# Kernel tuning notes

Measured on AMD Instinct MI355X. Metric: run time of the kernel, lower is better.

## Reference

```python
import math
import jax, jax.numpy as jnp
import numpy as np

N_HEADS = 16
D_EMBED = 1024
D_HEAD = D_EMBED // N_HEADS


def setup_inputs() -> dict:
    key = jax.random.key(0)
    k1, k2, k3, k4, k5 = jax.random.split(key, 5)
    B, S, D = 4, 2048, D_EMBED
    scale = 1.0 / math.sqrt(D)
    return {
        "x": jax.random.normal(k1, (B, S, D), dtype=jnp.float32),
        "in_proj_w": jax.random.normal(k2, (3 * D, D), dtype=jnp.float32) * scale,
        "in_proj_b": jax.random.normal(k3, (3 * D,), dtype=jnp.float32) * 0.02,
        "out_proj_w": jax.random.normal(k4, (D, D), dtype=jnp.float32) * scale,
        "out_proj_b": jax.random.normal(k5, (D,), dtype=jnp.float32) * 0.02,
        "causal_mask": 0,
    }


def reference(x, in_proj_w, in_proj_b, out_proj_w, out_proj_b, causal_mask):
    B, S, D = x.shape
    # in_proj: torch Linear -> x @ W^T + b, then chunk into q,k,v
    qkv = x @ in_proj_w.T + in_proj_b              # [B,S,3D]
    q, k, v = jnp.split(qkv, 3, axis=-1)
    # [B,S,D] -> [B,H,S,d]
    def heads(t):
        return t.reshape(B, S, N_HEADS, D_HEAD).transpose(0, 2, 1, 3)
    q, k, v = heads(q), heads(k), heads(v)
    weight = jnp.einsum("bhsd,bhtd->bhst", q, k)   # [B,H,S,S] materialized scores
    if causal_mask:
        mask = jnp.triu(jnp.ones((S, S), dtype=bool), k=1)
        weight = jnp.where(mask, -jnp.inf, weight)
    weight = jax.nn.softmax(weight / math.sqrt(D_HEAD), axis=-1)
    out = jnp.einsum("bhst,bhtd->bhsd", weight, v)  # [B,H,S,d]
    out = out.transpose(0, 2, 1, 3).reshape(B, S, D)
    return out @ out_proj_w.T + out_proj_b
```

## Files before the change

kernel.cpp:

```cpp
#include <hip/hip_runtime.h>

typedef unsigned short u16;
typedef _Float16 h8 __attribute__((ext_vector_type(8)));
typedef __fp16 fp16x2 __attribute__((ext_vector_type(2)));
typedef float f32x4 __attribute__((ext_vector_type(4)));

constexpr int B_ = 4, S_ = 2048, D_ = 1024, H_ = 16;

__device__ __forceinline__ void async16(const void* g, void* l) {
  __builtin_amdgcn_global_load_lds(
      (const __attribute__((address_space(1))) void*)g,
      (__attribute__((address_space(3))) void*)l, 16, 0, 0);
}

__device__ __forceinline__ unsigned pk2(float a, float b) {
  union { fp16x2 h; unsigned u; } c;
  c.h = __builtin_amdgcn_cvt_pkrtz(a, b);
  return c.u;
}

__global__ __launch_bounds__(256) void cvt3_kernel(
    const float* __restrict__ x, const float* __restrict__ wi,
    const float* __restrict__ wo, _Float16* __restrict__ xh,
    _Float16* __restrict__ wih, _Float16* __restrict__ woh)
{
  const int bid = blockIdx.x;
  const float* src;
  _Float16* dst;
  int base;
  if (bid < 8192)       { src = x;  dst = xh;  base = bid; }
  else if (bid < 11264) { src = wi; dst = wih; base = bid - 8192; }
  else                  { src = wo; dst = woh; base = bid - 11264; }
  const int i = (base * 256 + threadIdx.x) * 4;
  const float4 v = *(const float4*)(src + i);
  uint2 o;
  o.x = pk2(v.x, v.y);
  o.y = pk2(v.z, v.w);
  *(uint2*)(dst + i) = o;
}

template<bool OUT_HALF, int BPW>
__global__ __launch_bounds__(512, 2) void gemm256d_f16(
    const _Float16* __restrict__ A, const _Float16* __restrict__ Bw,
    const float* __restrict__ bias, void* __restrict__ Cout,
    int M, int N, int K)
{
  constexpr int BN = BPW * 64;
  constexpr int NBB = BN / 8;
  __shared__ __align__(16) _Float16 sA[2][16384];
  __shared__ __align__(16) _Float16 sB[2][NBB * 512];

  const int tid = threadIdx.x;
  const int lane = tid & 63, w = tid >> 6;
  const int wm = w >> 2, wn = w & 3;

  const int id = blockIdx.x;
  const int cpx = gridDim.x >> 3;
  const int swz = (id & 7) * cpx + (id >> 3);
  const int nbx = N / BN;
  const int bx = swz % nbx, by = swz / nbx;
  const int m0 = by * 256, n0 = bx * BN;

  const int r15 = lane & 15, s4 = lane >> 4;
  const _Float16* gA[4];
  int loA[4];
#pragma unroll
  for (int j = 0; j < 4; ++j) {
    const int t = 2 * w + (j >> 1), kk = j & 1;
    gA[j] = A + (size_t)(m0 + 16 * t + r15) * K + kk * 32 + s4 * 8;
    loA[j] = (t * 2 + kk) * 512;
  }
  const _Float16* gB[BPW];
  int loB[BPW];
#pragma unroll
  for (int j = 0; j < BPW; ++j) {
    const int f = w * BPW + j, nt = f >> 1, kk = f & 1;
    gB[j] = Bw + (size_t)(n0 + 16 * nt + r15) * K + kk * 32 + s4 * 8;
    loB[j] = f * 512;
  }

  const f32x4 zf = {0.f, 0.f, 0.f, 0.f};
  f32x4 acc[8][BPW];
#pragma unroll
  for (int i = 0; i < 8; ++i)
#pragma unroll
    for (int j = 0; j < BPW; ++j) acc[i][j] = zf;

#pragma unroll
  for (int j = 0; j < 4; ++j) async16(gA[j], &sA[0][loA[j]]);
#pragma unroll
  for (int j = 0; j < BPW; ++j) async16(gB[j], &sB[0][loB[j]]);
#pragma unroll
  for (int j = 0; j < 4; ++j) async16(gA[j] + 64, &sA[1][loA[j]]);
#pragma unroll
  for (int j = 0; j < BPW; ++j) async16(gB[j] + 64, &sB[1][loB[j]]);
  if constexpr (BPW == 4) asm volatile("s_waitcnt vmcnt(8)" ::: "memory");
  else                    asm volatile("s_waitcnt vmcnt(7)" ::: "memory");
  __builtin_amdgcn_s_barrier();

  const int NT = K >> 6;
  int cur = 0;
  for (int kt = 0; kt < NT; ++kt) {
    const _Float16* pA = sA[cur];
    const _Float16* pB = sB[cur];
    _Float16* nA = sA[cur];
    _Float16* nB = sB[cur];
    const bool st = (kt + 2 < NT);
    const int ko = (kt + 2) * 64;

    h8 fb[BPW][2];
#pragma unroll
    for (int p = 0; p < 4; ++p) {
      if (p == 0) {
#pragma unroll
        for (int nt = 0; nt < BPW; ++nt)
#pragma unroll
          for (int kk = 0; kk < 2; ++kk)
            fb[nt][kk] = *(const h8*)&pB[((wn * BPW + nt) * 2 + kk) * 512 + lane * 8];
      } else if (st) {
        if (p == 1) {
#pragma unroll
          for (int j = 0; j < BPW; ++j) async16(gB[j] + ko, &nB[loB[j]]);
        }
        if ((w & 3) == p - 1) {
#pragma unroll
          for (int j = 0; j < 4; ++j) async16(gA[j] + ko, &nA[loA[j]]);
        }
      }
      h8 fa[2][2];
#pragma unroll
      for (int i = 0; i < 2; ++i)
#pragma unroll
        for (int kk = 0; kk < 2; ++kk)
          fa[i][kk] = *(const h8*)&pA[((wm * 8 + 2 * p + i) * 2 + kk) * 512 + lane * 8];
      __builtin_amdgcn_s_setprio(1);
#pragma unroll
      for (int i = 0; i < 2; ++i)
#pragma unroll
        for (int nt = 0; nt < BPW; ++nt)
#pragma unroll
          for (int kk = 0; kk < 2; ++kk)
            acc[2 * p + i][nt] = __builtin_amdgcn_mfma_f32_16x16x32_f16(
                fa[i][kk], fb[nt][kk], acc[2 * p + i][nt], 0, 0, 0);
      __builtin_amdgcn_s_setprio(0);
      __builtin_amdgcn_s_barrier();
    }
    if (st && (w & 3) == 3) {
#pragma unroll
      for (int j = 0; j < 4; ++j) async16(gA[j] + ko, &nA[loA[j]]);
    }
    if (kt + 1 < NT) {
      if (st) {
        if constexpr (BPW == 4) asm volatile("s_waitcnt vmcnt(8)" ::: "memory");
        else                    asm volatile("s_waitcnt vmcnt(7)" ::: "memory");
      } else {
        asm volatile("s_waitcnt vmcnt(0)" ::: "memory");
      }
      __builtin_amdgcn_s_barrier();
    }
    cur ^= 1;
  }

  const int g = lane >> 4, cc = lane & 15;
#pragma unroll
  for (int nt = 0; nt < BPW; ++nt) {
    const int col = n0 + wn * (16 * BPW) + nt * 16 + cc;
    const float bv = bias[col];
#pragma unroll
    for (int mt = 0; mt < 8; ++mt) {
      const int rowb = m0 + wm * 128 + mt * 16 + g * 4;
#pragma unroll
      for (int r = 0; r < 4; ++r) {
        const float v = acc[mt][nt][r] + bv;
        if constexpr (OUT_HALF)
          ((_Float16*)Cout)[(size_t)(rowb + r) * N + col] = (_Float16)v;
        else
          ((float*)Cout)[(size_t)(rowb + r) * N + col] = v;
      }
    }
  }
}

template<bool OUT_HALF>
__global__ __launch_bounds__(256) void gemm_f16(
    const _Float16* __restrict__ A, const _Float16* __restrict__ Bw,
    const float* __restrict__ bias, void* __restrict__ Cout,
    int M, int N, int K)
{
  __shared__ __align__(16) _Float16 sA[4096];
  __shared__ __align__(16) _Float16 sB[4096];

  const int tid = threadIdx.x;
  const int lane = tid & 63, w = tid >> 6;
  const int wm = w & 1, wn = w >> 1;
  const int m0 = blockIdx.y * 128, n0 = blockIdx.x * 128;

  const int sr = 16 * w + (lane & 15);
  const int ss = lane >> 4;
  const _Float16* gA1 = A + (size_t)(m0 + sr) * K + 8 * ss;
  const _Float16* gA2 = gA1 + (size_t)64 * K;
  const _Float16* gB1 = Bw + (size_t)(n0 + sr) * K + 8 * ss;
  const _Float16* gB2 = gB1 + (size_t)64 * K;
  _Float16* lA1 = &sA[w * 512];
  _Float16* lA2 = &sA[(w + 4) * 512];
  _Float16* lB1 = &sB[w * 512];
  _Float16* lB2 = &sB[(w + 4) * 512];

  const f32x4 zf = {0.f, 0.f, 0.f, 0.f};
  f32x4 acc[4][4];
#pragma unroll
  for (int i = 0; i < 4; ++i)
#pragma unroll
    for (int j = 0; j < 4; ++j) acc[i][j] = zf;

  for (int k0 = 0; k0 < K; k0 += 32) {
    __syncthreads();
    async16(gA1 + k0, lA1);
    async16(gA2 + k0, lA2);
    async16(gB1 + k0, lB1);
    async16(gB2 + k0, lB2);
    __syncthreads();

    h8 fa[4], fb[4];
#pragma unroll
    for (int i = 0; i < 4; ++i) {
      fa[i] = *(const h8*)&sA[((wm * 4 + i) << 9) + (lane << 3)];
      fb[i] = *(const h8*)&sB[((wn * 4 + i) << 9) + (lane << 3)];
    }
#pragma unroll
    for (int i = 0; i < 4; ++i)
#pragma unroll
      for (int j = 0; j < 4; ++j)
        acc[i][j] = __builtin_amdgcn_mfma_f32_16x16x32_f16(fa[i], fb[j], acc[i][j], 0, 0, 0);
  }

  const int g = lane >> 4, cc = lane & 15;
#pragma unroll
  for (int j = 0; j < 4; ++j) {
    const int col = n0 + (wn * 4 + j) * 16 + cc;
    const float bv = bias[col];
#pragma unroll
    for (int i = 0; i < 4; ++i) {
      const int rowb = m0 + (wm * 4 + i) * 16 + g * 4;
#pragma unroll
      for (int r = 0; r < 4; ++r) {
        const float v = acc[i][j][r] + bv;
        if constexpr (OUT_HALF)
          ((_Float16*)Cout)[(size_t)(rowb + r) * N + col] = (_Float16)v;
        else
          ((float*)Cout)[(size_t)(rowb + r) * N + col] = v;
      }
    }
  }
}

__global__ __launch_bounds__(256) void transpose_v(
    const u16* __restrict__ qkv, u16* __restrict__ vT)
{
  __shared__ u16 T[64 * 73];
  const int tid = threadIdx.x;
  const int bh = blockIdx.y, s0 = blockIdx.x * 64;
  const int b = bh >> 4, h = bh & 15;
#pragma unroll
  for (int t = 0; t < 2; ++t) {
    const int c = tid + t * 256, r = c >> 3, cs = c & 7;
    union { int4 v; u16 s[8]; } u;
    u.v = *(const int4*)(qkv + (size_t)(b * S_ + s0 + r) * 3072 + 2048 + h * 64 + 8 * cs);
#pragma unroll
    for (int i = 0; i < 8; ++i) T[r * 73 + 8 * cs + i] = u.s[i];
  }
  __syncthreads();
#pragma unroll
  for (int t = 0; t < 2; ++t) {
    const int c = tid + t * 256, rd = c >> 3, ss = c & 7;
    union { int4 v; u16 s[8]; } u;
#pragma unroll
    for (int i = 0; i < 8; ++i) u.s[i] = T[(8 * ss + i) * 73 + rd];
    *(int4*)(vT + (size_t)(bh * 64 + rd) * S_ + s0 + 8 * ss) = u.v;
  }
}

__global__ __launch_bounds__(256, 4) void attn_f16(
    const _Float16* __restrict__ qkv, const _Float16* __restrict__ vT,
    _Float16* __restrict__ attnO, const int* __restrict__ causal_ptr)
{
  __shared__ __align__(16) _Float16 sQP[9216];
  __shared__ __align__(16) _Float16 sK[4096];
  __shared__ __align__(16) _Float16 sV[4096];

  const int tid = threadIdx.x, lane = tid & 63, w = tid >> 6;
  const int q4 = lane >> 4, cc = lane & 15;
  const int bh = blockIdx.y, b = bh >> 4, h = bh & 15;
  const int q0 = blockIdx.x * 128;
  const int causal = causal_ptr[0];

  {
    const int rr = lane & 15, sc8 = lane >> 4;
#pragma unroll
    for (int tt = 0; tt < 2; ++tt) {
      const int t = 2 * w + tt;
#pragma unroll
      for (int sh = 0; sh < 2; ++sh) {
        const _Float16* g = qkv + (size_t)(b * S_ + q0 + 16 * t + rr) * 3072 + h * 64 + 8 * (4 * sh + sc8);
        async16(g, &sQP[t * 1024 + sh * 512]);
      }
    }
  }
  __syncthreads();

  h8 qf[2][2];
#pragma unroll
  for (int m = 0; m < 2; ++m)
#pragma unroll
    for (int kk = 0; kk < 2; ++kk) {
      h8 v = *(const h8*)&sQP[((2 * w + m) << 10) + (kk << 9) + (lane << 3)];
      qf[m][kk] = v * (_Float16)0.125f;
    }

  h8 ones;
#pragma unroll
  for (int i = 0; i < 8; ++i) ones[i] = (_Float16)1.0f;

  const _Float16* gK = qkv + (size_t)(b * S_ + 16 * w + (lane & 15)) * 3072 + 1024 + h * 64 + 8 * (lane >> 4);
  const _Float16* gV = vT + (size_t)(bh * 64 + 16 * w + (lane & 15)) * S_ + 8 * (lane >> 4);
  _Float16* lK0 = &sK[w * 1024];
  _Float16* lV0 = &sV[w * 1024];

  const int wp = w * 2304;

  const f32x4 zf = {0.f, 0.f, 0.f, 0.f};
  f32x4 oa[2][4], lac[2];
#pragma unroll
  for (int m = 0; m < 2; ++m) {
    lac[m] = zf;
#pragma unroll
    for (int nt = 0; nt < 4; ++nt) oa[m][nt] = zf;
  }

  for (int j0 = 0; j0 < S_; j0 += 64) {
    if (causal && j0 > q0 + 127) break;
    __syncthreads();
    async16(gK + (size_t)j0 * 3072, lK0);
    async16(gK + (size_t)j0 * 3072 + 32, lK0 + 512);
    async16(gV + j0, lV0);
    async16(gV + j0 + 32, lV0 + 512);
    __syncthreads();

    f32x4 sc[2][4];
#pragma unroll
    for (int nt = 0; nt < 4; ++nt) {
      const h8 kf0 = *(const h8*)&sK[(nt << 10) + (lane << 3)];
      const h8 kf1 = *(const h8*)&sK[(nt << 10) + 512 + (lane << 3)];
#pragma unroll
      for (int m = 0; m < 2; ++m) {
        sc[m][nt] = __builtin_amdgcn_mfma_f32_16x16x32_f16(kf0, qf[m][0], zf, 0, 0, 0);
        sc[m][nt] = __builtin_amdgcn_mfma_f32_16x16x32_f16(kf1, qf[m][1], sc[m][nt], 0, 0, 0);
      }
    }

    if (causal) {
#pragma unroll
      for (int m = 0; m < 2; ++m)
#pragma unroll
        for (int nt = 0; nt < 4; ++nt)
#pragma unroll
          for (int r = 0; r < 4; ++r)
            if ((j0 + nt * 16 + q4 * 4 + r) > (q0 + 32 * w + m * 16 + cc))
              sc[m][nt][r] = -1.0e30f;
    }

#pragma unroll
    for (int m = 0; m < 2; ++m)
#pragma unroll
      for (int nt = 0; nt < 4; ++nt) {
        uint2 pk;
        pk.x = pk2(__expf(sc[m][nt][0]), __expf(sc[m][nt][1]));
        pk.y = pk2(__expf(sc[m][nt][2]), __expf(sc[m][nt][3]));
        *(uint2*)&sQP[wp + (m * 16 + cc) * 72 + nt * 16 + q4 * 4] = pk;
      }

    asm volatile("s_waitcnt lgkmcnt(0)" ::: "memory");

    h8 pf[2][2];
#pragma unroll
    for (int m = 0; m < 2; ++m)
#pragma unroll
      for (int kk = 0; kk < 2; ++kk)
        pf[m][kk] = *(const h8*)&sQP[wp + (m * 16 + cc) * 72 + kk * 32 + q4 * 8];

#pragma unroll
    for (int m = 0; m < 2; ++m) {
      lac[m] = __builtin_amdgcn_mfma_f32_16x16x32_f16(pf[m][0], ones, lac[m], 0, 0, 0);
      lac[m] = __builtin_amdgcn_mfma_f32_16x16x32_f16(pf[m][1], ones, lac[m], 0, 0, 0);
    }
#pragma unroll
    for (int nt = 0; nt < 4; ++nt) {
      const h8 vf0 = *(const h8*)&sV[(nt << 10) + (lane << 3)];
      const h8 vf1 = *(const h8*)&sV[(nt << 10) + 512 + (lane << 3)];
#pragma unroll
      for (int m = 0; m < 2; ++m) {
        oa[m][nt] = __builtin_amdgcn_mfma_f32_16x16x32_f16(pf[m][0], vf0, oa[m][nt], 0, 0, 0);
        oa[m][nt] = __builtin_amdgcn_mfma_f32_16x16x32_f16(pf[m][1], vf1, oa[m][nt], 0, 0, 0);
      }
    }
  }

#pragma unroll
  for (int m = 0; m < 2; ++m) {
    float inv[4];
#pragma unroll
    for (int r = 0; r < 4; ++r) inv[r] = 1.0f / lac[m][r];
#pragma unroll
    for (int nt = 0; nt < 4; ++nt) {
      const int col = h * 64 + nt * 16 + cc;
#pragma unroll
      for (int r = 0; r < 4; ++r) {
        const int row = b * S_ + q0 + 32 * w + m * 16 + q4 * 4 + r;
        attnO[(size_t)row * D_ + col] = (_Float16)(oa[m][nt][r] * inv[r]);
      }
    }
  }
}

extern "C" void kernel_launch(void* const* d_in, const int* in_sizes, int n_in,
                              void* d_out, int out_size, void* d_ws, size_t ws_size,
                              hipStream_t stream)
{
  const float* x  = (const float*)d_in[0];
  const float* wi = (const float*)d_in[1];
  const float* bi = (const float*)d_in[2];
  const float* wo = (const float*)d_in[3];
  const float* bo = (const float*)d_in[4];
  const int* causal = (const int*)d_in[5];

  _Float16* xh   = (_Float16*)d_ws;
  _Float16* wih  = xh + 8388608;
  _Float16* woh  = wih + 3145728;
  _Float16* qkvb = woh + 1048576;
  _Float16* vT   = qkvb + 25165824;
  _Float16* attn = vT + 8388608;

  const int M = B_ * S_;

  cvt3_kernel<<<12288, 256, 0, stream>>>(x, wi, wo, xh, wih, woh);

  gemm256d_f16<true, 3><<<512, 512, 0, stream>>>(
      xh, wih, bi, qkvb, M, 3 * D_, D_);

  transpose_v<<<dim3(32, 64), 256, 0, stream>>>((const u16*)qkvb, (u16*)vT);

  attn_f16<<<dim3(16, 64), 256, 0, stream>>>(qkvb, vT, attn, causal);

  gemm_f16<false><<<dim3(8, 64), 256, 0, stream>>>(
      attn, woh, bo, d_out, M, D_, D_);
}
```

Measured before the change: 311.1 us.

## Fold softmax scale into QKV epilogue, use exp2, reuse big GEMM for out-proj

The softmax scale and the log2(e) factor are folded into the Q columns in the QKV GEMM epilogue, and the attention kernel now uses a native exp2 instead of __expf. This removes the per-element Q rescale and the extra multiply inside exp. The simple 128x128 out-projection GEMM is replaced by the pipelined 256-row double-buffered GEMM with BPW=2, with new wait counts for that width. MFMA sections in attention get raised wave priority via s_setprio. Rounding Q to fp16 after pre-scaling changes numerics slightly.

```diff
diff --git a/kernel.cpp b/kernel.cpp
--- a/kernel.cpp
+++ b/kernel.cpp
@@ -18,6 +18,16 @@
   c.h = __builtin_amdgcn_cvt_pkrtz(a, b);
   return c.u;
 }
+
+__device__ __forceinline__ float fexp2(float x) {
+#if __has_builtin(__builtin_amdgcn_exp2f)
+  return __builtin_amdgcn_exp2f(x);
+#else
+  return exp2f(x);
+#endif
+}
+
+#define QSCALE 0.18033688011112042f
 
 __global__ __launch_bounds__(256) void cvt3_kernel(
     const float* __restrict__ x, const float* __restrict__ wi,
@@ -39,7 +49,7 @@
   *(uint2*)(dst + i) = o;
 }
 
-template<bool OUT_HALF, int BPW>
+template<bool OUT_HALF, int BPW, bool SCALE_Q>
 __global__ __launch_bounds__(512, 2) void gemm256d_f16(
     const _Float16* __restrict__ A, const _Float16* __restrict__ Bw,
     const float* __restrict__ bias, void* __restrict__ Cout,
@@ -94,8 +104,9 @@
   for (int j = 0; j < 4; ++j) async16(gA[j] + 64, &sA[1][loA[j]]);
 #pragma unroll
   for (int j = 0; j < BPW; ++j) async16(gB[j] + 64, &sB[1][loB[j]]);
-  if constexpr (BPW == 4) asm volatile("s_waitcnt vmcnt(8)" ::: "memory");
-  else                    asm volatile("s_waitcnt vmcnt(7)" ::: "memory");
+  if constexpr (BPW == 2)      asm volatile("s_waitcnt vmcnt(6)" ::: "memory");
+  else if constexpr (BPW == 3) asm volatile("s_waitcnt vmcnt(7)" ::: "memory");
+  else                         asm volatile("s_waitcnt vmcnt(8)" ::: "memory");
   __builtin_amdgcn_s_barrier();
 
   const int NT = K >> 6;
@@ -151,8 +162,9 @@
     }
     if (kt + 1 < NT) {
       if (st) {
-        if constexpr (BPW == 4) asm volatile("s_waitcnt vmcnt(8)" ::: "memory");
-        else                    asm volatile("s_waitcnt vmcnt(7)" ::: "memory");
+        if constexpr (BPW == 2)      asm volatile("s_waitcnt vmcnt(6)" ::: "memory");
+        else if constexpr (BPW == 3) asm volatile("s_waitcnt vmcnt(7)" ::: "memory");
+        else                         asm volatile("s_waitcnt vmcnt(8)" ::: "memory");
       } else {
         asm volatile("s_waitcnt vmcnt(0)" ::: "memory");
       }
@@ -166,85 +178,15 @@
   for (int nt = 0; nt < BPW; ++nt) {
     const int col = n0 + wn * (16 * BPW) + nt * 16 + cc;
     const float bv = bias[col];
+    float qs = 1.0f;
+    if constexpr (SCALE_Q) qs = (col < 1024) ? QSCALE : 1.0f;
 #pragma unroll
     for (int mt = 0; mt < 8; ++mt) {
       const int rowb = m0 + wm * 128 + mt * 16 + g * 4;
 #pragma unroll
       for (int r = 0; r < 4; ++r) {
-        const float v = acc[mt][nt][r] + bv;
-        if constexpr (OUT_HALF)
-          ((_Float16*)Cout)[(size_t)(rowb + r) * N + col] = (_Float16)v;
-        else
-          ((float*)Cout)[(size_t)(rowb + r) * N + col] = v;
-      }
-    }
-  }
-}
-
-template<bool OUT_HALF>
-__global__ __launch_bounds__(256) void gemm_f16(
-    const _Float16* __restrict__ A, const _Float16* __restrict__ Bw,
-    const float* __restrict__ bias, void* __restrict__ Cout,
-    int M, int N, int K)
-{
-  __shared__ __align__(16) _Float16 sA[4096];
-  __shared__ __align__(16) _Float16 sB[4096];
-
-  const int tid = threadIdx.x;
-  const int lane = tid & 63, w = tid >> 6;
-  const int wm = w & 1, wn = w >> 1;
-  const int m0 = blockIdx.y * 128, n0 = blockIdx.x * 128;
-
-  const int sr = 16 * w + (lane & 15);
-  const int ss = lane >> 4;
-  const _Float16* gA1 = A + (size_t)(m0 + sr) * K + 8 * ss;
-  const _Float16* gA2 = gA1 + (size_t)64 * K;
-  const _Float16* gB1 = Bw + (size_t)(n0 + sr) * K + 8 * ss;
-  const _Float16* gB2 = gB1 + (size_t)64 * K;
-  _Float16* lA1 = &sA[w * 512];
-  _Float16* lA2 = &sA[(w + 4) * 512];
-  _Float16* lB1 = &sB[w * 512];
-  _Float16* lB2 = &sB[(w + 4) * 512];
-
-  const f32x4 zf = {0.f, 0.f, 0.f, 0.f};
-  f32x4 acc[4][4];
-#pragma unroll
-  for (int i = 0; i < 4; ++i)
-#pragma unroll
-    for (int j = 0; j < 4; ++j) acc[i][j] = zf;
-
-  for (int k0 = 0; k0 < K; k0 += 32) {
-    __syncthreads();
-    async16(gA1 + k0, lA1);
-    async16(gA2 + k0, lA2);
-    async16(gB1 + k0, lB1);
-    async16(gB2 + k0, lB2);
-    __syncthreads();
-
-    h8 fa[4], fb[4];
-#pragma unroll
-    for (int i = 0; i < 4; ++i) {
-      fa[i] = *(const h8*)&sA[((wm * 4 + i) << 9) + (lane << 3)];
-      fb[i] = *(const h8*)&sB[((wn * 4 + i) << 9) + (lane << 3)];
-    }
-#pragma unroll
-    for (int i = 0; i < 4; ++i)
-#pragma unroll
-      for (int j = 0; j < 4; ++j)
-        acc[i][j] = __builtin_amdgcn_mfma_f32_16x16x32_f16(fa[i], fb[j], acc[i][j], 0, 0, 0);
-  }
-
-  const int g = lane >> 4, cc = lane & 15;
-#pragma unroll
-  for (int j = 0; j < 4; ++j) {
-    const int col = n0 + (wn * 4 + j) * 16 + cc;
-    const float bv = bias[col];
-#pragma unroll
-    for (int i = 0; i < 4; ++i) {
-      const int rowb = m0 + (wm * 4 + i) * 16 + g * 4;
-#pragma unroll
-      for (int r = 0; r < 4; ++r) {
-        const float v = acc[i][j][r] + bv;
+        float v = acc[mt][nt][r] + bv;
+        if constexpr (SCALE_Q) v *= qs;
         if constexpr (OUT_HALF)
           ((_Float16*)Cout)[(size_t)(rowb + r) * N + col] = (_Float16)v;
         else
@@ -312,10 +254,8 @@
 #pragma unroll
   for (int m = 0; m < 2; ++m)
 #pragma unroll
-    for (int kk = 0; kk < 2; ++kk) {
-      h8 v = *(const h8*)&sQP[((2 * w + m) << 10) + (kk << 9) + (lane << 3)];
-      qf[m][kk] = v * (_Float16)0.125f;
-    }
+    for (int kk = 0; kk < 2; ++kk)
+      qf[m][kk] = *(const h8*)&sQP[((2 * w + m) << 10) + (kk << 9) + (lane << 3)];
 
   h8 ones;
 #pragma unroll
@@ -347,6 +287,7 @@
     __syncthreads();
 
     f32x4 sc[2][4];
+    __builtin_amdgcn_s_setprio(1);
 #pragma unroll
     for (int nt = 0; nt < 4; ++nt) {
       const h8 kf0 = *(const h8*)&sK[(nt << 10) + (lane << 3)];
@@ -357,6 +298,7 @@
         sc[m][nt] = __builtin_amdgcn_mfma_f32_16x16x32_f16(kf1, qf[m][1], sc[m][nt], 0, 0, 0);
       }
     }
+    __builtin_amdgcn_s_setprio(0);
 
     if (causal) {
 #pragma unroll
@@ -374,8 +316,8 @@
 #pragma unroll
       for (int nt = 0; nt < 4; ++nt) {
         uint2 pk;
-        pk.x = pk2(__expf(sc[m][nt][0]), __expf(sc[m][nt][1]));
-        pk.y = pk2(__expf(sc[m][nt][2]), __expf(sc[m][nt][3]));
+        pk.x = pk2(fexp2(sc[m][nt][0]), fexp2(sc[m][nt][1]));
+        pk.y = pk2(fexp2(sc[m][nt][2]), fexp2(sc[m][nt][3]));
         *(uint2*)&sQP[wp + (m * 16 + cc) * 72 + nt * 16 + q4 * 4] = pk;
       }
 
@@ -388,6 +330,7 @@
       for (int kk = 0; kk < 2; ++kk)
         pf[m][kk] = *(const h8*)&sQP[wp + (m * 16 + cc) * 72 + kk * 32 + q4 * 8];
 
+    __builtin_amdgcn_s_setprio(1);
 #pragma unroll
     for (int m = 0; m < 2; ++m) {
       lac[m] = __builtin_amdgcn_mfma_f32_16x16x32_f16(pf[m][0], ones, lac[m], 0, 0, 0);
@@ -403,6 +346,7 @@
         oa[m][nt] = __builtin_amdgcn_mfma_f32_16x16x32_f16(pf[m][1], vf1, oa[m][nt], 0, 0, 0);
       }
     }
+    __builtin_amdgcn_s_setprio(0);
   }
 
 #pragma unroll
@@ -444,13 +388,13 @@
 
   cvt3_kernel<<<12288, 256, 0, stream>>>(x, wi, wo, xh, wih, woh);
 
-  gemm256d_f16<true, 3><<<512, 512, 0, stream>>>(
+  gemm256d_f16<true, 3, true><<<512, 512, 0, stream>>>(
       xh, wih, bi, qkvb, M, 3 * D_, D_);
 
   transpose_v<<<dim3(32, 64), 256, 0, stream>>>((const u16*)qkvb, (u16*)vT);
 
   attn_f16<<<dim3(16, 64), 256, 0, stream>>>(qkvb, vT, attn, causal);
 
-  gemm_f16<false><<<dim3(8, 64), 256, 0, stream>>>(
+  gemm256d_f16<false, 2, false><<<256, 512, 0, stream>>>(
       attn, woh, bo, d_out, M, D_, D_);
 }
```

After: 311.7 us. About the same (+0.2%).
